# Kernel tuning notes

Hardware: AMD Instinct MI355X
Metric: run time of the kernel (lower is better)

The kernel has to match this reference:

```python
import jax, jax.numpy as jnp
import numpy as np

B, S, DIM, H, DH = 2, 2048, 1024, 16, 64
INNER = H * DH


def setup_inputs() -> dict:
    key = jax.random.key(0)
    ks = jax.random.split(key, 4)
    sd = 0.02
    return {
        "x": jax.random.normal(ks[0], (B, S, DIM), dtype=jnp.float32),
        "ln_w": jnp.ones((DIM,), jnp.float32),
        "ln_b": jnp.zeros((DIM,), jnp.float32),
        "Wq": jax.random.normal(ks[1], (DIM, INNER), jnp.float32) * sd,
        "Wkv": jax.random.normal(ks[2], (DIM, 2 * INNER), jnp.float32) * sd,
        "q_gamma": jnp.ones((H, 1, DH), jnp.float32),
        "k_gamma": jnp.ones((H, 1, DH), jnp.float32),
        "Wo": jax.random.normal(ks[3], (INNER, DIM), jnp.float32) * sd,
    }


def _rmsnorm(t, gamma, scale):
    # t: (b,h,s,d); gamma: (h,1,d)
    normed = t * jax.lax.rsqrt(jnp.mean(t * t, axis=-1, keepdims=True) + 1e-8)
    return normed * scale * gamma


def reference(x, ln_w, ln_b, Wq, Wkv, q_gamma, k_gamma, Wo):
    h, dh = q_gamma.shape[0], q_gamma.shape[-1]
    b, s, _ = x.shape
    # pre-LayerNorm (eps 1e-5, biased variance)
    mean = jnp.mean(x, axis=-1, keepdims=True)
    var = jnp.var(x, axis=-1, keepdims=True)
    xn = ln_w * (x - mean) / jnp.sqrt(var + 1e-5) + ln_b
    # projections
    q = xn @ Wq                       # (b,s,h*dh)
    k, v = jnp.split(xn @ Wkv, 2, axis=-1)
    # split heads -> (b,h,s,dh)
    to_heads = lambda t: t.reshape(b, s, h, dh).transpose(0, 2, 1, 3)
    q, k, v = to_heads(q), to_heads(k), to_heads(v)
    scale = dh ** 0.5
    q = _rmsnorm(q, q_gamma, scale)
    k = _rmsnorm(k, k_gamma, scale)
    # attention (no extra 1/sqrt(d): RMSNorm scale already applied)
    dots = jnp.einsum("bhid,bhjd->bhij", q, k)
    attn = jax.nn.softmax(dots, axis=-1)
    out = jnp.einsum("bhij,bhjd->bhid", attn, v)
    out = out.transpose(0, 2, 1, 3).reshape(b, s, h * dh)
    return out @ Wo
```

## Files before the change

kernel.cpp:

```cpp
#include <hip/hip_runtime.h>
#include <hip/hip_bf16.h>

#define DEVFN __device__ __forceinline__

typedef __attribute__((ext_vector_type(8))) short short8;
typedef __attribute__((ext_vector_type(4))) short short4v;
typedef __attribute__((ext_vector_type(4))) float f32x4;

#define MFMA(a,b,c) __builtin_amdgcn_mfma_f32_16x16x32_bf16((a),(b),(c),0,0,0)

DEVFN void gload_lds16(const __hip_bfloat16* g, __hip_bfloat16* l) {
  __builtin_amdgcn_global_load_lds((const __attribute__((address_space(1))) void*)g,
                                   (__attribute__((address_space(3))) void*)l, 16, 0, 0);
}

DEVFN float bf2f(__hip_bfloat16 h) { return __bfloat162float(h); }
DEVFN __hip_bfloat16 f2bf(float f) { return __float2bfloat16(f); }

DEVFN void store_out(float* p, float v) { *p = v; }
DEVFN void store_out(__hip_bfloat16* p, float v) { *p = f2bf(v); }

__global__ __launch_bounds__(256) void ln_split_kernel(
    const float* __restrict__ x, const float* __restrict__ lw, const float* __restrict__ lb,
    __hip_bfloat16* __restrict__ xh, __hip_bfloat16* __restrict__ xl) {
  int row = blockIdx.x, t = threadIdx.x;
  float4 v = ((const float4*)(x + (size_t)row * 1024))[t];
  float s  = v.x + v.y + v.z + v.w;
  float ss = v.x*v.x + v.y*v.y + v.z*v.z + v.w*v.w;
  #pragma unroll
  for (int m = 1; m < 64; m <<= 1) { s += __shfl_xor(s, m); ss += __shfl_xor(ss, m); }
  __shared__ float red[8];
  int wv = t >> 6;
  if ((t & 63) == 0) { red[wv] = s; red[4 + wv] = ss; }
  __syncthreads();
  s  = red[0] + red[1] + red[2] + red[3];
  ss = red[4] + red[5] + red[6] + red[7];
  float mean = s * (1.f/1024.f);
  float var  = ss * (1.f/1024.f) - mean*mean;
  float inv  = rsqrtf(var + 1e-5f);
  float4 wv4 = ((const float4*)lw)[t];
  float4 bv4 = ((const float4*)lb)[t];
  float xv[4] = {v.x, v.y, v.z, v.w};
  float wa[4] = {wv4.x, wv4.y, wv4.z, wv4.w};
  float ba[4] = {bv4.x, bv4.y, bv4.z, bv4.w};
  union { short4v s4; __hip_bfloat16 h[4]; } uh, ul;
  #pragma unroll
  for (int j = 0; j < 4; ++j) {
    float val = (xv[j] - mean) * inv * wa[j] + ba[j];
    __hip_bfloat16 hi = f2bf(val);
    uh.h[j] = hi;
    ul.h[j] = f2bf(val - bf2f(hi));
  }
  ((short4v*)(xh + (size_t)row * 1024))[t] = uh.s4;
  ((short4v*)(xl + (size_t)row * 1024))[t] = ul.s4;
}

__global__ __launch_bounds__(256) void wprep_kernel(
    const float* __restrict__ Wq, const float* __restrict__ Wkv, const float* __restrict__ Wo,
    __hip_bfloat16* __restrict__ Wqk_h, __hip_bfloat16* __restrict__ Wqk_l,
    __hip_bfloat16* __restrict__ Wv, __hip_bfloat16* __restrict__ Wot) {
  __shared__ float tile[64][68];
  int bid = blockIdx.x, t = threadIdx.x;
  const float* src; int srcN, kt, nt, drow;
  __hip_bfloat16 *dh, *dl;
  if (bid < 256) {
    src = Wq; srcN = 1024; kt = bid >> 4; nt = bid & 15;
    dh = Wqk_h; dl = Wqk_l; drow = nt * 64;
  } else if (bid < 768) {
    int r = bid - 256; src = Wkv; srcN = 2048; kt = r >> 5; nt = r & 31;
    if (nt < 16) { dh = Wqk_h; dl = Wqk_l; drow = 1024 + nt * 64; }
    else         { dh = Wv;    dl = nullptr; drow = (nt - 16) * 64; }
  } else {
    int r = bid - 768; src = Wo; srcN = 1024; kt = r >> 4; nt = r & 15;
    dh = Wot; dl = nullptr; drow = nt * 64;
  }
  int lr = t >> 2, c = t & 3;
  const float* sp = src + (size_t)(kt*64 + lr) * srcN + nt*64 + c*16;
  float* tr = &tile[lr][c*16];
  ((float4*)tr)[0] = ((const float4*)sp)[0];
  ((float4*)tr)[1] = ((const float4*)sp)[1];
  ((float4*)tr)[2] = ((const float4*)sp)[2];
  ((float4*)tr)[3] = ((const float4*)sp)[3];
  __syncthreads();
  union { short8 s8[2]; __hip_bfloat16 h[16]; } hh, ll;
  #pragma unroll
  for (int e = 0; e < 16; ++e) {
    float wv = tile[c*16 + e][lr];
    __hip_bfloat16 hi = f2bf(wv);
    hh.h[e] = hi;
    ll.h[e] = f2bf(wv - bf2f(hi));
  }
  size_t doff = (size_t)(drow + lr) * 1024 + kt*64 + c*16;
  ((short8*)(dh + doff))[0] = hh.s8[0];
  ((short8*)(dh + doff))[1] = hh.s8[1];
  if (dl) {
    ((short8*)(dl + doff))[0] = ll.s8[0];
    ((short8*)(dl + doff))[1] = ll.s8[1];
  }
}

__global__ __launch_bounds__(256) void gemm_dual_kernel(
    const __hip_bfloat16* __restrict__ Ah, const __hip_bfloat16* __restrict__ Al,
    const __hip_bfloat16* __restrict__ Bh, const __hip_bfloat16* __restrict__ Bl,
    __hip_bfloat16* __restrict__ Ch, __hip_bfloat16* __restrict__ Cl,
    const float* __restrict__ qg, const float* __restrict__ kg) {
  __shared__ __align__(16) __hip_bfloat16 sAh[128*32], sAl[128*32], sBh[128*32], sBl[128*32];
  const int K = 1024, N = 2048;
  int mt = blockIdx.x, nt = blockIdx.y;
  int t = threadIdx.x, w = t >> 6, l = t & 63;
  int wr = w >> 1, wc = w & 1, lr = l & 15, lk = (l >> 4) * 8;
  f32x4 acc[4][4] = {};
  for (int k0 = 0; k0 < K; k0 += 32) {
    #pragma unroll
    for (int i = 0; i < 2; ++i) {
      int ci = i*256 + t;
      size_t ga = (size_t)(mt*128 + (ci >> 2)) * K + k0 + (ci & 3) * 8;
      size_t gb = (size_t)(nt*128 + (ci >> 2)) * K + k0 + (ci & 3) * 8;
      int ldst = (i*256 + w*64) * 8;
      gload_lds16(Ah + ga, sAh + ldst);
      gload_lds16(Al + ga, sAl + ldst);
      gload_lds16(Bh + gb, sBh + ldst);
      gload_lds16(Bl + gb, sBl + ldst);
    }
    __syncthreads();
    short8 ah[4], al[4], bh[4], bl[4];
    #pragma unroll
    for (int m = 0; m < 4; ++m) {
      int ro = (wr*64 + m*16 + lr)*32 + lk;
      ah[m] = *(const short8*)(sAh + ro);
      al[m] = *(const short8*)(sAl + ro);
    }
    #pragma unroll
    for (int n = 0; n < 4; ++n) {
      int ro = (wc*64 + n*16 + lr)*32 + lk;
      bh[n] = *(const short8*)(sBh + ro);
      bl[n] = *(const short8*)(sBl + ro);
    }
    #pragma unroll
    for (int m = 0; m < 4; ++m)
      #pragma unroll
      for (int n = 0; n < 4; ++n) {
        acc[m][n] = MFMA(ah[m], bh[n], acc[m][n]);
        acc[m][n] = MFMA(ah[m], bl[n], acc[m][n]);
        acc[m][n] = MFMA(al[m], bh[n], acc[m][n]);
      }
    __syncthreads();
  }
  int col0 = nt*128 + wc*64;
  int head = col0 >> 6;
  const float* gamma = (head < 16) ? (qg + head*64) : (kg + (head - 16)*64);
  float g[4];
  #pragma unroll
  for (int nf = 0; nf < 4; ++nf) g[nf] = gamma[nf*16 + lr];
  #pragma unroll
  for (int m = 0; m < 4; ++m) {
    #pragma unroll
    for (int r = 0; r < 4; ++r) {
      float ss2 = 0.f;
      #pragma unroll
      for (int nf = 0; nf < 4; ++nf) ss2 += acc[m][nf][r] * acc[m][nf][r];
      #pragma unroll
      for (int msk = 1; msk < 16; msk <<= 1) ss2 += __shfl_xor(ss2, msk);
      float scl = rsqrtf(ss2 * (1.f/64.f) + 1e-8f) * 8.f;
      int row = mt*128 + wr*64 + m*16 + (l >> 4)*4 + r;
      #pragma unroll
      for (int nf = 0; nf < 4; ++nf) {
        float val = acc[m][nf][r] * scl * g[nf];
        __hip_bfloat16 hi = f2bf(val);
        size_t off = (size_t)row * N + col0 + nf*16 + lr;
        Ch[off] = hi;
        Cl[off] = f2bf(val - bf2f(hi));
      }
    }
  }
}

template <typename OUT_T>
__global__ __launch_bounds__(256) void gemm_single_kernel(
    const __hip_bfloat16* __restrict__ A, const __hip_bfloat16* __restrict__ Bt,
    OUT_T* __restrict__ C, int N) {
  __shared__ __align__(16) __hip_bfloat16 sA[128*32], sB[128*32];
  const int K = 1024;
  int mt = blockIdx.x, nt = blockIdx.y;
  int t = threadIdx.x, w = t >> 6, l = t & 63;
  int wr = w >> 1, wc = w & 1, lr = l & 15, lk = (l >> 4) * 8;
  f32x4 acc[4][4] = {};
  for (int k0 = 0; k0 < K; k0 += 32) {
    #pragma unroll
    for (int i = 0; i < 2; ++i) {
      int ci = i*256 + t;
      size_t ga = (size_t)(mt*128 + (ci >> 2)) * K + k0 + (ci & 3) * 8;
      size_t gb = (size_t)(nt*128 + (ci >> 2)) * K + k0 + (ci & 3) * 8;
      int ldst = (i*256 + w*64) * 8;
      gload_lds16(A + ga, sA + ldst);
      gload_lds16(Bt + gb, sB + ldst);
    }
    __syncthreads();
    short8 af[4], bf[4];
    #pragma unroll
    for (int m = 0; m < 4; ++m) af[m] = *(const short8*)(sA + (wr*64 + m*16 + lr)*32 + lk);
    #pragma unroll
    for (int n = 0; n < 4; ++n) bf[n] = *(const short8*)(sB + (wc*64 + n*16 + lr)*32 + lk);
    #pragma unroll
    for (int m = 0; m < 4; ++m)
      #pragma unroll
      for (int n = 0; n < 4; ++n)
        acc[m][n] = MFMA(af[m], bf[n], acc[m][n]);
    __syncthreads();
  }
  int row0 = mt*128 + wr*64, col0 = nt*128 + wc*64;
  #pragma unroll
  for (int m = 0; m < 4; ++m)
    #pragma unroll
    for (int n = 0; n < 4; ++n)
      #pragma unroll
      for (int r = 0; r < 4; ++r) {
        int row = row0 + m*16 + (l >> 4)*4 + r;
        int col = col0 + n*16 + lr;
        store_out(&C[(size_t)row * N + col], acc[m][n][r]);
      }
}

__global__ __launch_bounds__(256) void vtrans_kernel(
    const __hip_bfloat16* __restrict__ vbuf, __hip_bfloat16* __restrict__ vT) {
  __shared__ __hip_bfloat16 tile[64][72];
  int bid = blockIdx.x;
  int b = bid >> 9, h = (bid >> 5) & 15, st = bid & 31;
  int t = threadIdx.x, j = t >> 2, c = t & 3;
  const short8* src = (const short8*)(vbuf + (size_t)(b*2048 + st*64 + j) * 1024 + h*64 + c*16);
  *(short8*)&tile[j][c*16]     = src[0];
  *(short8*)&tile[j][c*16 + 8] = src[1];
  __syncthreads();
  int d = t >> 2, c2 = t & 3;
  union { short8 s8[2]; __hip_bfloat16 hh[16]; } o;
  #pragma unroll
  for (int e = 0; e < 16; ++e) o.hh[e] = tile[c2*16 + e][d];
  short8* dst = (short8*)(vT + (size_t)((b*16 + h)*64 + d) * 2048 + st*64 + c2*16);
  dst[0] = o.s8[0];
  dst[1] = o.s8[1];
}

__global__ __launch_bounds__(256) void attn_kernel(
    const __hip_bfloat16* __restrict__ qk_h, const __hip_bfloat16* __restrict__ qk_l,
    const __hip_bfloat16* __restrict__ vT, __hip_bfloat16* __restrict__ ao) {
  __shared__ __align__(16) __hip_bfloat16 sKh[2][4096], sKl[2][4096], sVt[2][4096];
  __shared__ __align__(16) __hip_bfloat16 sP[4096];
  int t = threadIdx.x, w = t >> 6, l = t & 63, lr = l & 15, hi = l >> 4, lk = hi * 8;
  int bh = blockIdx.x & 31, qt = blockIdx.x >> 5;
  int b = bh >> 4, h = bh & 15;
  const __hip_bfloat16* qbh = qk_h + (size_t)b * 2048 * 2048 + h * 64;
  const __hip_bfloat16* qbl = qk_l + (size_t)b * 2048 * 2048 + h * 64;
  const __hip_bfloat16* kbh = qbh + 1024;
  const __hip_bfloat16* kbl = qbl + 1024;
  const __hip_bfloat16* vtb = vT + (size_t)bh * 64 * 2048;
  int qrow = qt*64 + w*16 + lr;
  short8 qh0 = *(const short8*)(qbh + (size_t)qrow*2048 + lk);
  short8 qh1 = *(const short8*)(qbh + (size_t)qrow*2048 + 32 + lk);
  short8 ql0 = *(const short8*)(qbl + (size_t)qrow*2048 + lk);
  short8 ql1 = *(const short8*)(qbl + (size_t)qrow*2048 + 32 + lk);
  f32x4 o_acc[4] = {};
  f32x4 l_acc = {0.f, 0.f, 0.f, 0.f};
  float m_run[4];
  #pragma unroll
  for (int r = 0; r < 4; ++r) m_run[r] = -1e30f;
  const short8 ones = {0x3F80, 0x3F80, 0x3F80, 0x3F80, 0x3F80, 0x3F80, 0x3F80, 0x3F80};

  int swl = lr & 7;
  int c0e = (hi ^ swl) << 3;
  int c1e = c0e ^ 32;
  int ci0 = t, ci1 = 256 + t;
  int r0 = ci0 >> 3, cs0 = (ci0 & 7) ^ (r0 & 7);
  int r1 = ci1 >> 3, cs1 = (ci1 & 7) ^ (r1 & 7);
  int ldb0 = (w*64) * 8, ldb1 = (256 + w*64) * 8;

#define STAGE(B, KV) do { \
    gload_lds16(kbh + (size_t)((KV) + r0)*2048 + cs0*8, &sKh[B][0] + ldb0); \
    gload_lds16(kbh + (size_t)((KV) + r1)*2048 + cs1*8, &sKh[B][0] + ldb1); \
    gload_lds16(kbl + (size_t)((KV) + r0)*2048 + cs0*8, &sKl[B][0] + ldb0); \
    gload_lds16(kbl + (size_t)((KV) + r1)*2048 + cs1*8, &sKl[B][0] + ldb1); \
    gload_lds16(vtb + (size_t)r0*2048 + (KV) + cs0*8, &sVt[B][0] + ldb0); \
    gload_lds16(vtb + (size_t)r1*2048 + (KV) + cs1*8, &sVt[B][0] + ldb1); \
  } while (0)

  STAGE(0, 0);
  int buf = 0;
  for (int tile = 0; tile < 32; ++tile) {
    int kv0 = tile << 6;
    if (tile < 31) {
      STAGE(buf ^ 1, kv0 + 64);
      asm volatile("s_waitcnt vmcnt(6)" ::: "memory");
    } else {
      asm volatile("s_waitcnt vmcnt(0)" ::: "memory");
    }
    __builtin_amdgcn_s_barrier();
    const __hip_bfloat16* pKh = &sKh[buf][0];
    const __hip_bfloat16* pKl = &sKl[buf][0];
    const __hip_bfloat16* pVt = &sVt[buf][0];
    f32x4 s_acc[4];
    __builtin_amdgcn_s_setprio(1);
    #pragma unroll
    for (int nf = 0; nf < 4; ++nf) {
      int rb = (nf*16 + lr) * 64;
      short8 kh0 = *(const short8*)(pKh + rb + c0e);
      short8 kh1 = *(const short8*)(pKh + rb + c1e);
      short8 kl0 = *(const short8*)(pKl + rb + c0e);
      short8 kl1 = *(const short8*)(pKl + rb + c1e);
      f32x4 sa = {};
      sa = MFMA(qh0, kh0, sa);
      sa = MFMA(qh1, kh1, sa);
      sa = MFMA(qh0, kl0, sa);
      sa = MFMA(qh1, kl1, sa);
      sa = MFMA(ql0, kh0, sa);
      sa = MFMA(ql1, kh1, sa);
      s_acc[nf] = sa;
    }
    __builtin_amdgcn_s_setprio(0);
    #pragma unroll
    for (int r = 0; r < 4; ++r) {
      float mx = fmaxf(fmaxf(s_acc[0][r], s_acc[1][r]), fmaxf(s_acc[2][r], s_acc[3][r]));
      #pragma unroll
      for (int msk = 1; msk < 16; msk <<= 1) mx = fmaxf(mx, __shfl_xor(mx, msk));
      if (!__all(mx <= m_run[r] + 8.f)) {
        float mnew = fmaxf(m_run[r], mx);
        float corr = __expf(m_run[r] - mnew);
        m_run[r] = mnew;
        #pragma unroll
        for (int df = 0; df < 4; ++df) o_acc[df][r] *= corr;
        l_acc[r] *= corr;
      }
      int prow = hi*4 + r;
      int pbase = (w << 10) + prow*64 + swl;
      #pragma unroll
      for (int nf = 0; nf < 4; ++nf) {
        float pv = __expf(s_acc[nf][r] - m_run[r]);
        int chunk = (nf << 1) | (lr >> 3);
        sP[pbase + ((chunk ^ (prow & 7)) << 3)] = f2bf(pv);
      }
    }
    __builtin_amdgcn_s_setprio(1);
    #pragma unroll
    for (int kk = 0; kk < 2; ++kk) {
      int vck = (((kk << 2) | hi) ^ swl) << 3;
      short8 pf = *(const short8*)(sP + (w << 10) + lr*64 + vck);
      l_acc = MFMA(pf, ones, l_acc);
      #pragma unroll
      for (int df = 0; df < 4; ++df) {
        short8 vf = *(const short8*)(pVt + (df*16 + lr)*64 + vck);
        o_acc[df] = MFMA(pf, vf, o_acc[df]);
      }
    }
    __builtin_amdgcn_s_setprio(0);
    __builtin_amdgcn_s_barrier();
    buf ^= 1;
  }
#undef STAGE
  size_t orow0 = (size_t)b*2048 + qt*64 + w*16 + hi*4;
  #pragma unroll
  for (int df = 0; df < 4; ++df)
    #pragma unroll
    for (int r = 0; r < 4; ++r) {
      float oval = o_acc[df][r] / l_acc[r];
      ao[(orow0 + r) * 1024 + h*64 + df*16 + lr] = f2bf(oval);
    }
}

extern "C" void kernel_launch(void* const* d_in, const int* in_sizes, int n_in,
                              void* d_out, int out_size, void* d_ws, size_t ws_size,
                              hipStream_t stream) {
  const float* x   = (const float*)d_in[0];
  const float* lw  = (const float*)d_in[1];
  const float* lb  = (const float*)d_in[2];
  const float* Wq  = (const float*)d_in[3];
  const float* Wkv = (const float*)d_in[4];
  const float* qg  = (const float*)d_in[5];
  const float* kg  = (const float*)d_in[6];
  const float* Wo  = (const float*)d_in[7];
  float* out = (float*)d_out;
  char* ws = (char*)d_ws;
  const size_t MB = 1024 * 1024;
  __hip_bfloat16* xh    = (__hip_bfloat16*)(ws + 0);
  __hip_bfloat16* xl    = (__hip_bfloat16*)(ws + 8*MB);
  __hip_bfloat16* qk_h  = (__hip_bfloat16*)(ws + 16*MB);
  __hip_bfloat16* qk_l  = (__hip_bfloat16*)(ws + 32*MB);
  __hip_bfloat16* Wqk_h = (__hip_bfloat16*)(ws + 48*MB);
  __hip_bfloat16* Wqk_l = (__hip_bfloat16*)(ws + 52*MB);
  __hip_bfloat16* Wv    = (__hip_bfloat16*)(ws + 56*MB);
  __hip_bfloat16* Wot   = (__hip_bfloat16*)(ws + 58*MB);
  __hip_bfloat16* vT    = (__hip_bfloat16*)(ws + 60*MB);
  __hip_bfloat16* vbuf  = (__hip_bfloat16*)(ws + 8*MB);
  __hip_bfloat16* ao    = (__hip_bfloat16*)(ws + 0);

  ln_split_kernel<<<4096, 256, 0, stream>>>(x, lw, lb, xh, xl);
  wprep_kernel<<<1024, 256, 0, stream>>>(Wq, Wkv, Wo, Wqk_h, Wqk_l, Wv, Wot);
  gemm_dual_kernel<<<dim3(32, 16), 256, 0, stream>>>(xh, xl, Wqk_h, Wqk_l, qk_h, qk_l, qg, kg);
  gemm_single_kernel<__hip_bfloat16><<<dim3(32, 8), 256, 0, stream>>>(xh, Wv, vbuf, 1024);
  vtrans_kernel<<<1024, 256, 0, stream>>>(vbuf, vT);
  attn_kernel<<<1024, 256, 0, stream>>>(qk_h, qk_l, vT, ao);
  gemm_single_kernel<float><<<dim3(32, 8), 256, 0, stream>>>(ao, Wot, out, 1024);
}
```

Before: 328.3 us.

## Keep P in registers via transposed QK MFMA and load V directly to registers

Swaps the MFMA operand order so each lane owns one query column of S. The softmax max then needs only two cross-lane shuffles and P can be packed and shuffled into A-operand layout without going through LDS. V^T tiles are now loaded straight from global into registers each tile instead of being staged in LDS. This removes the sP and sVt shared buffers and their LDS traffic, at the cost of more shuffles, more registers, and V global loads that are not prefetched a full tile ahead.

```diff
diff --git a/kernel.cpp b/kernel.cpp
--- a/kernel.cpp
+++ b/kernel.cpp
@@ -243,8 +243,7 @@
 __global__ __launch_bounds__(256) void attn_kernel(
     const __hip_bfloat16* __restrict__ qk_h, const __hip_bfloat16* __restrict__ qk_l,
     const __hip_bfloat16* __restrict__ vT, __hip_bfloat16* __restrict__ ao) {
-  __shared__ __align__(16) __hip_bfloat16 sKh[2][4096], sKl[2][4096], sVt[2][4096];
-  __shared__ __align__(16) __hip_bfloat16 sP[4096];
+  __shared__ __align__(16) __hip_bfloat16 sKh[2][4096], sKl[2][4096];
   int t = threadIdx.x, w = t >> 6, l = t & 63, lr = l & 15, hi = l >> 4, lk = hi * 8;
   int bh = blockIdx.x & 31, qt = blockIdx.x >> 5;
   int b = bh >> 4, h = bh & 15;
@@ -260,17 +259,14 @@
   short8 ql1 = *(const short8*)(qbl + (size_t)qrow*2048 + 32 + lk);
   f32x4 o_acc[4] = {};
   f32x4 l_acc = {0.f, 0.f, 0.f, 0.f};
-  float m_run[4];
-  #pragma unroll
-  for (int r = 0; r < 4; ++r) m_run[r] = -1e30f;
+  float m_run = -1e30f;
   const short8 ones = {0x3F80, 0x3F80, 0x3F80, 0x3F80, 0x3F80, 0x3F80, 0x3F80, 0x3F80};
 
   int swl = lr & 7;
   int c0e = (hi ^ swl) << 3;
   int c1e = c0e ^ 32;
-  int ci0 = t, ci1 = 256 + t;
-  int r0 = ci0 >> 3, cs0 = (ci0 & 7) ^ (r0 & 7);
-  int r1 = ci1 >> 3, cs1 = (ci1 & 7) ^ (r1 & 7);
+  int r0 = t >> 3, cs0 = (t & 7) ^ (r0 & 7);
+  int r1 = 32 + r0, cs1 = (t & 7) ^ (r1 & 7);
   int ldb0 = (w*64) * 8, ldb1 = (256 + w*64) * 8;
 
 #define STAGE(B, KV) do { \
@@ -278,24 +274,27 @@
     gload_lds16(kbh + (size_t)((KV) + r1)*2048 + cs1*8, &sKh[B][0] + ldb1); \
     gload_lds16(kbl + (size_t)((KV) + r0)*2048 + cs0*8, &sKl[B][0] + ldb0); \
     gload_lds16(kbl + (size_t)((KV) + r1)*2048 + cs1*8, &sKl[B][0] + ldb1); \
-    gload_lds16(vtb + (size_t)r0*2048 + (KV) + cs0*8, &sVt[B][0] + ldb0); \
-    gload_lds16(vtb + (size_t)r1*2048 + (KV) + cs1*8, &sVt[B][0] + ldb1); \
   } while (0)
 
   STAGE(0, 0);
   int buf = 0;
   for (int tile = 0; tile < 32; ++tile) {
     int kv0 = tile << 6;
+    short8 vreg[4][2];
+    #pragma unroll
+    for (int df = 0; df < 4; ++df)
+      #pragma unroll
+      for (int kk = 0; kk < 2; ++kk)
+        vreg[df][kk] = *(const short8*)(vtb + (size_t)(df*16 + lr)*2048 + kv0 + kk*32 + lk);
     if (tile < 31) {
       STAGE(buf ^ 1, kv0 + 64);
-      asm volatile("s_waitcnt vmcnt(6)" ::: "memory");
+      asm volatile("s_waitcnt vmcnt(12)" ::: "memory");
     } else {
-      asm volatile("s_waitcnt vmcnt(0)" ::: "memory");
+      asm volatile("s_waitcnt vmcnt(8)" ::: "memory");
     }
     __builtin_amdgcn_s_barrier();
     const __hip_bfloat16* pKh = &sKh[buf][0];
     const __hip_bfloat16* pKl = &sKl[buf][0];
-    const __hip_bfloat16* pVt = &sVt[buf][0];
     f32x4 s_acc[4];
     __builtin_amdgcn_s_setprio(1);
     #pragma unroll
@@ -306,48 +305,65 @@
       short8 kl0 = *(const short8*)(pKl + rb + c0e);
       short8 kl1 = *(const short8*)(pKl + rb + c1e);
       f32x4 sa = {};
-      sa = MFMA(qh0, kh0, sa);
-      sa = MFMA(qh1, kh1, sa);
-      sa = MFMA(qh0, kl0, sa);
-      sa = MFMA(qh1, kl1, sa);
-      sa = MFMA(ql0, kh0, sa);
-      sa = MFMA(ql1, kh1, sa);
+      sa = MFMA(kh0, qh0, sa);
+      sa = MFMA(kh1, qh1, sa);
+      sa = MFMA(kl0, qh0, sa);
+      sa = MFMA(kl1, qh1, sa);
+      sa = MFMA(kh0, ql0, sa);
+      sa = MFMA(kh1, ql1, sa);
       s_acc[nf] = sa;
     }
     __builtin_amdgcn_s_setprio(0);
-    #pragma unroll
-    for (int r = 0; r < 4; ++r) {
-      float mx = fmaxf(fmaxf(s_acc[0][r], s_acc[1][r]), fmaxf(s_acc[2][r], s_acc[3][r]));
-      #pragma unroll
-      for (int msk = 1; msk < 16; msk <<= 1) mx = fmaxf(mx, __shfl_xor(mx, msk));
-      if (!__all(mx <= m_run[r] + 8.f)) {
-        float mnew = fmaxf(m_run[r], mx);
-        float corr = __expf(m_run[r] - mnew);
-        m_run[r] = mnew;
+    float mx = s_acc[0][0];
+    #pragma unroll
+    for (int nf = 0; nf < 4; ++nf)
+      #pragma unroll
+      for (int r = 0; r < 4; ++r) mx = fmaxf(mx, s_acc[nf][r]);
+    mx = fmaxf(mx, __shfl_xor(mx, 16));
+    mx = fmaxf(mx, __shfl_xor(mx, 32));
+    if (!__all(mx <= m_run + 8.f)) {
+      float mnew = fmaxf(m_run, mx);
+      float corr = __expf(m_run - mnew);
+      m_run = mnew;
+      float corrq[4];
+      #pragma unroll
+      for (int r = 0; r < 4; ++r) corrq[r] = __shfl(corr, hi*4 + r);
+      #pragma unroll
+      for (int r = 0; r < 4; ++r) {
+        l_acc[r] *= corrq[r];
         #pragma unroll
-        for (int df = 0; df < 4; ++df) o_acc[df][r] *= corr;
-        l_acc[r] *= corr;
+        for (int df = 0; df < 4; ++df) o_acc[df][r] *= corrq[r];
       }
-      int prow = hi*4 + r;
-      int pbase = (w << 10) + prow*64 + swl;
-      #pragma unroll
-      for (int nf = 0; nf < 4; ++nf) {
-        float pv = __expf(s_acc[nf][r] - m_run[r]);
-        int chunk = (nf << 1) | (lr >> 3);
-        sP[pbase + ((chunk ^ (prow & 7)) << 3)] = f2bf(pv);
+    }
+    unsigned long long quad[4];
+    #pragma unroll
+    for (int nf = 0; nf < 4; ++nf) {
+      union { unsigned long long u; unsigned short us[4]; } pk;
+      #pragma unroll
+      for (int r = 0; r < 4; ++r) {
+        float pv = __expf(s_acc[nf][r] - m_run);
+        __hip_bfloat16 pb = f2bf(pv);
+        pk.us[r] = *(unsigned short*)&pb;
       }
+      quad[nf] = pk.u;
     }
     __builtin_amdgcn_s_setprio(1);
     #pragma unroll
     for (int kk = 0; kk < 2; ++kk) {
-      int vck = (((kk << 2) | hi) ^ swl) << 3;
-      short8 pf = *(const short8*)(sP + (w << 10) + lr*64 + vck);
+      unsigned long long q0 = quad[2*kk], q1 = quad[2*kk + 1];
+      int srcA = lr + ((hi & 1) << 5);
+      unsigned long long a0 = __shfl(q0, srcA);
+      unsigned long long a1 = __shfl(q1, srcA);
+      unsigned long long b0 = __shfl(q0, srcA + 16);
+      unsigned long long b1 = __shfl(q1, srcA + 16);
+      union { short8 s8; unsigned long long u[2]; } pfu;
+      pfu.u[0] = (hi & 2) ? a1 : a0;
+      pfu.u[1] = (hi & 2) ? b1 : b0;
+      short8 pf = pfu.s8;
       l_acc = MFMA(pf, ones, l_acc);
       #pragma unroll
-      for (int df = 0; df < 4; ++df) {
-        short8 vf = *(const short8*)(pVt + (df*16 + lr)*64 + vck);
-        o_acc[df] = MFMA(pf, vf, o_acc[df]);
-      }
+      for (int df = 0; df < 4; ++df)
+        o_acc[df] = MFMA(pf, vreg[df][kk], o_acc[df]);
     }
     __builtin_amdgcn_s_setprio(0);
     __builtin_amdgcn_s_barrier();
```

Result: slower. 362.6 us (+10.5%).
